# Performance work log

Measured on AMD Instinct MI355X. Metric: run time of the kernel, lower is better.

## Reference

```python
import jax, jax.numpy as jnp
import numpy as np

ZETA = 1.03
GAMMA = -0.03


def setup_inputs() -> dict:
    key = jax.random.key(0)
    k1, k2, k3 = jax.random.split(key, 3)
    B, S, H, D = 2, 2048, 16, 128
    return {
        "query_states": jax.random.normal(k1, (B * S, H, D), dtype=jnp.float32),
        "key_states": jax.random.normal(k2, (B * S, H, D), dtype=jnp.float32),
        "value_states": jax.random.normal(k3, (B * S, H, D), dtype=jnp.float32),
        "batch_size": B,
        "q_length": S,
        "kv_length": S,
    }


def reference(query_states, key_states, value_states, batch_size, q_length, kv_length):
    H = query_states.shape[1]
    D = query_states.shape[2]
    # [B*S, H, D] -> [B, S, H, D]
    q = query_states.reshape(batch_size, q_length, H, D)
    k = key_states.reshape(batch_size, kv_length, H, D)
    v = value_states.reshape(batch_size, kv_length, H, D)
    # scores: [B, H, Q, K]
    scores = jnp.einsum("bqhd,bkhd->bhqk", q, k) / jnp.sqrt(jnp.float32(D)).astype(q.dtype)
    causal = jnp.triu(jnp.ones((q_length, kv_length), dtype=bool), k=1)  # True above diagonal
    scores = jnp.where(causal[None, None, :, :], -jnp.inf, scores)
    probs = jax.nn.softmax(scores, axis=-1)
    # clipped softmax (fp8 recipe): clip((zeta-gamma)*p + gamma, 0, 1)
    probs = jnp.clip((ZETA - GAMMA) * probs + GAMMA, 0.0, 1.0)
    out = jnp.einsum("bhqk,bkhd->bqhd", probs, v)
    return out.reshape(batch_size * q_length, H, D)
```

## Files before the change

kernel.cpp:

```cpp
#include <hip/hip_runtime.h>

typedef __attribute__((ext_vector_type(4))) float f32x4;
typedef __attribute__((ext_vector_type(8))) short bf16x8;
typedef __attribute__((ext_vector_type(4))) int   i32x4;
typedef __attribute__((ext_vector_type(2))) int   i32x2;

#define B_ 2
#define S_ 2048
#define H_ 16
#define D_ 128
#define RS_ (H_ * D_)
#define LOG2E 1.44269504088896340736f
#define ZG 1.06f
#define GM (-0.03f)
#define QSC (0.08838834764831845f * LOG2E)

__device__ __forceinline__ ushort f2bf(float x) {
    uint u = __builtin_bit_cast(uint, x);
    u += 0x7FFFu + ((u >> 16) & 1u);
    return (ushort)(u >> 16);
}

__device__ __forceinline__ void gld16(const void* g, void* l) {
    __builtin_amdgcn_global_load_lds(
        (const __attribute__((address_space(1))) unsigned int*)g,
        (__attribute__((address_space(3))) unsigned int*)l, 16, 0, 0);
}

__global__ __launch_bounds__(256)
void prep_kv(const float* __restrict__ Kg, const float* __restrict__ Vg,
             ushort* __restrict__ Kb, ushort* __restrict__ Vt)
{
    __shared__ ushort Vl[64 * 136];
    const int t = threadIdx.x;
    if (blockIdx.x < 512) {
        const int n  = blockIdx.x;
        const int bh = n >> 4;
        const int ch = n & 15;
        const int s  = ch * 128 + (t >> 1);
        const int d0 = (t & 1) * 64;
        const int b  = bh >> 4, h = bh & 15;
        const float* in = Kg + (((size_t)b * S_ + s) * H_ + h) * D_ + d0;
        ushort* out = Kb + ((size_t)bh * S_ + s) * D_ + d0;
#pragma unroll
        for (int j = 0; j < 4; ++j) {
            f32x4 x0 = *(const f32x4*)(in + j * 16);
            f32x4 x1 = *(const f32x4*)(in + j * 16 + 4);
            f32x4 x2 = *(const f32x4*)(in + j * 16 + 8);
            f32x4 x3 = *(const f32x4*)(in + j * 16 + 12);
            union { ushort u[16]; i32x4 v[2]; } p;
#pragma unroll
            for (int i = 0; i < 4; ++i) {
                p.u[i]      = f2bf(x0[i]);
                p.u[4 + i]  = f2bf(x1[i]);
                p.u[8 + i]  = f2bf(x2[i]);
                p.u[12 + i] = f2bf(x3[i]);
            }
            *(i32x4*)(out + j * 16)     = p.v[0];
            *(i32x4*)(out + j * 16 + 8) = p.v[1];
        }
    } else {
        const int n  = blockIdx.x - 512;
        const int bh = n >> 5;
        const int kt = n & 31;
        const int b  = bh >> 4, h = bh & 15;
#pragma unroll
        for (int it = 0; it < 2; ++it) {
            const int r  = it * 32 + (t >> 3);
            const int c0 = (t & 7) * 16;
            const int s  = kt * 64 + r;
            const float* in = Vg + (((size_t)b * S_ + s) * H_ + h) * D_ + c0;
            f32x4 x0 = *(const f32x4*)(in);
            f32x4 x1 = *(const f32x4*)(in + 4);
            f32x4 x2 = *(const f32x4*)(in + 8);
            f32x4 x3 = *(const f32x4*)(in + 12);
            union { ushort u[16]; i32x4 v[2]; } p;
#pragma unroll
            for (int i = 0; i < 4; ++i) {
                p.u[i]      = f2bf(x0[i]);
                p.u[4 + i]  = f2bf(x1[i]);
                p.u[8 + i]  = f2bf(x2[i]);
                p.u[12 + i] = f2bf(x3[i]);
            }
            *(i32x4*)(Vl + r * 136 + c0)     = p.v[0];
            *(i32x4*)(Vl + r * 136 + c0 + 8) = p.v[1];
        }
        __syncthreads();
        const int d  = t >> 1;
        const int kh = (t & 1) * 32;
        ushort* out = Vt + ((size_t)bh * 32 + kt) * 8192 + d * 64 + kh;
        uint wds[16];
#pragma unroll
        for (int i = 0; i < 16; ++i) {
            uint a = Vl[(kh + 2 * i) * 136 + d];
            uint c = Vl[(kh + 2 * i + 1) * 136 + d];
            wds[i] = a | (c << 16);
        }
#pragma unroll
        for (int j = 0; j < 4; ++j)
            *(i32x4*)(out + j * 8) = *(i32x4*)&wds[j * 4];
    }
}

__global__ __launch_bounds__(256, 3)
void attn_one(const float* __restrict__ Qg, const ushort* __restrict__ Kb,
              const ushort* __restrict__ Vt, float* __restrict__ Og)
{
    __shared__ char SHc[32768 + 4 * 2304 + 4096 + 16];

    const int tid  = threadIdx.x;
    const int w    = tid >> 6;
    const int lane = tid & 63;
    const int g    = lane >> 4;
    const int l15  = lane & 15;
    char*  const Kl    = SHc;
    char*  const Vl    = SHc + 16384;
    char*  const pB    = SHc + 32768 + w * 2304;
    float* const SmaxL = (float*)(SHc + 41984);
    uint*  const Flags = (uint*)(SHc + 46080);

    const int n  = blockIdx.x;
    const int qt = 31 - (n >> 5);
    const int bh = n & 31;
    const int b  = bh >> 4, h = bh & 15;

    const int q0  = qt * 64;
    const int qw0 = q0 + w * 16;
    const int qme = qw0 + l15;

    const float*  Qbh = Qg + ((size_t)b * S_ * H_ + h) * D_;
    const ushort* Kp  = Kb + (size_t)bh * S_ * D_;
    const ushort* Vp  = Vt + (size_t)bh * 32 * 8192;

    auto stageK2 = [&](int kt) {
#pragma unroll
        for (int i = 0; i < 8; ++i) {
            const int u = (w * 8 + i) * 64 + lane;
            const int r = u >> 4, cc = u & 15;
            const ushort* src = Kp + (size_t)(kt * 128 + r) * 128 + ((cc ^ (r & 15)) * 8);
            gld16(src, SHc + (w * 8 + i) * 1024);
        }
    };
    auto stageKV = [&](int kt) {
#pragma unroll
        for (int i = 0; i < 4; ++i) {
            const int u = (w * 4 + i) * 64 + lane;
            const int r = u >> 4, cc = u & 15;
            const ushort* src = Kp + (size_t)(kt * 64 + r) * 128 + ((cc ^ (r & 15)) * 8);
            gld16(src, Kl + (w * 4 + i) * 1024);
        }
        const ushort* tile = Vp + (size_t)kt * 8192;
#pragma unroll
        for (int i = 0; i < 4; ++i) {
            const int u = (w * 4 + i) * 64 + lane;
            const int r = u >> 3, cc = u & 7;
            const ushort* src = tile + r * 64 + ((cc ^ (r & 7)) * 8);
            gld16(src, Vl + (w * 4 + i) * 1024);
        }
    };

    stageK2(0);

    bf16x8 qf[4];
    {
        const float* qptr = Qbh + (size_t)qme * RS_;
#pragma unroll
        for (int db = 0; db < 4; ++db) {
            const float* p = qptr + db * 32 + g * 8;
            f32x4 a = *(const f32x4*)p;
            f32x4 d = *(const f32x4*)(p + 4);
#pragma unroll
            for (int i = 0; i < 4; ++i) {
                qf[db][i]     = (short)f2bf(a[i] * QSC);
                qf[db][i + 4] = (short)f2bf(d[i] * QSC);
            }
        }
    }
    asm volatile("s_waitcnt vmcnt(0)" ::: "memory");
    __syncthreads();

    float acc = 0.f;
    const int kt1 = (q0 + 191) >> 7;
#pragma unroll 1
    for (int kt = 0; kt < kt1; ++kt) {
        const ushort* K2 = (const ushort*)SHc;
        f32x4 s[8];
#pragma unroll
        for (int cc = 0; cc < 8; ++cc) s[cc] = (f32x4){0.f, 0.f, 0.f, 0.f};
        __builtin_amdgcn_s_setprio(1);
#pragma unroll
        for (int db = 0; db < 4; ++db) {
            const int usw = ((db * 4 + g) ^ l15) * 8;
#pragma unroll
            for (int cc = 0; cc < 8; ++cc) {
                bf16x8 kf = *(const bf16x8*)(K2 + (cc * 16 + l15) * 128 + usw);
                s[cc] = __builtin_amdgcn_mfma_f32_16x16x32_bf16(kf, qf[db], s[cc], 0, 0, 0);
            }
        }
        __builtin_amdgcn_s_setprio(0);
        float sm = -1e30f;
        if (kt == kt1 - 1) {
#pragma unroll
            for (int cc = 0; cc < 8; ++cc) {
                const int key0 = kt * 128 + cc * 16 + g * 4;
#pragma unroll
                for (int r = 0; r < 4; ++r) {
                    const bool ok = (key0 + r <= qme);
                    const float e = exp2f(s[cc][r]);
                    acc += ok ? e : 0.f;
                    sm = fmaxf(sm, ok ? s[cc][r] : -1e30f);
                }
            }
        } else {
#pragma unroll
            for (int cc = 0; cc < 8; ++cc)
#pragma unroll
                for (int r = 0; r < 4; ++r) {
                    acc += exp2f(s[cc][r]);
                    sm = fmaxf(sm, s[cc][r]);
                }
        }
        sm = fmaxf(sm, __shfl_xor(sm, 16));
        sm = fmaxf(sm, __shfl_xor(sm, 32));
        if (lane < 16) SmaxL[(w * 16 + kt) * 16 + l15] = sm;
        __syncthreads();
        if (kt + 1 < kt1) {
            stageK2(kt + 1);
            asm volatile("s_waitcnt vmcnt(0)" ::: "memory");
        }
        __syncthreads();
    }

    float c1;
    {
        float t = acc;
        t += __shfl_xor(t, 16);
        t += __shfl_xor(t, 32);
        c1 = ZG / t;
    }
    const float thr = log2f(-GM / c1);

    uint mymask = 0;
#pragma unroll 1
    for (int st = 0; st < kt1; ++st) {
        const float sm = SmaxL[(w * 16 + st) * 16 + l15];
        if (__any(sm > thr)) mymask |= (1u << st);
    }
    if (lane == 0) Flags[w] = mymask;
    __syncthreads();
    const uint blockmask = Flags[0] | Flags[1] | Flags[2] | Flags[3];

    const int kt2 = qt + 1;
    int kt = 0;
    while (kt < kt2 && !((blockmask >> (kt >> 1)) & 1u)) ++kt;
    if (kt < kt2) stageKV(kt);
    asm volatile("s_waitcnt vmcnt(0)" ::: "memory");
    __syncthreads();

    f32x4 o[8];
#pragma unroll
    for (int db = 0; db < 8; ++db) o[db] = (f32x4){0.f, 0.f, 0.f, 0.f};

#pragma unroll 1
    while (kt < kt2) {
        f32x4 s[4];
#pragma unroll
        for (int cb = 0; cb < 4; ++cb) s[cb] = (f32x4){0.f, 0.f, 0.f, 0.f};
        __builtin_amdgcn_s_setprio(1);
#pragma unroll
        for (int db = 0; db < 4; ++db) {
            const int usw = ((db * 4 + g) ^ l15) * 8;
#pragma unroll
            for (int cb = 0; cb < 4; ++cb) {
                bf16x8 kf = *(const bf16x8*)((const ushort*)Kl + (cb * 16 + l15) * 128 + usw);
                s[cb] = __builtin_amdgcn_mfma_f32_16x16x32_bf16(kf, qf[db], s[cb], 0, 0, 0);
            }
        }
        __builtin_amdgcn_s_setprio(0);

        float smax = fmaxf(fmaxf(fmaxf(s[0][0], s[0][1]), fmaxf(s[0][2], s[0][3])),
                           fmaxf(fmaxf(s[1][0], s[1][1]), fmaxf(s[1][2], s[1][3])));
        smax = fmaxf(smax,
               fmaxf(fmaxf(fmaxf(s[2][0], s[2][1]), fmaxf(s[2][2], s[2][3])),
                     fmaxf(fmaxf(s[3][0], s[3][1]), fmaxf(s[3][2], s[3][3]))));

        if (__any(smax > thr)) {
            const bool diag = (kt == kt2 - 1);
#pragma unroll
            for (int cb = 0; cb < 4; ++cb) {
                const int key0 = kt * 64 + cb * 16 + g * 4;
                float p[4];
#pragma unroll
                for (int r = 0; r < 4; ++r) {
                    float e = exp2f(s[cb][r]);
                    if (diag) e = (key0 + r <= qme) ? e : 0.f;
                    p[r] = fminf(fmaxf(c1 * e + GM, 0.f), 1.f);
                }
                uint r01, r23;
                asm("v_cvt_pk_bf16_f32 %0, %1, %2" : "=v"(r01) : "v"(p[0]), "v"(p[1]));
                asm("v_cvt_pk_bf16_f32 %0, %1, %2" : "=v"(r23) : "v"(p[2]), "v"(p[3]));
                i32x2 pv2 = {(int)r01, (int)r23};
                *(i32x2*)(pB + l15 * 144 + cb * 32 + g * 8) = pv2;
            }
            asm volatile("s_waitcnt lgkmcnt(0)" ::: "memory");
            f32x4 onew[8];
            __builtin_amdgcn_s_setprio(1);
#pragma unroll
            for (int ks = 0; ks < 2; ++ks) {
                bf16x8 pf = *(const bf16x8*)(pB + l15 * 144 + ks * 64 + g * 16);
#pragma unroll
                for (int db = 0; db < 8; ++db) {
                    const int d = db * 16 + l15;
                    bf16x8 vf = *(const bf16x8*)(Vl + d * 128 +
                                                 (((ks * 4 + g) ^ (d & 7)) * 16));
                    f32x4& dst = (ks == 0) ? onew[db] : o[db];
                    const f32x4 src = (ks == 0) ? o[db] : onew[db];
                    dst = __builtin_amdgcn_mfma_f32_16x16x32_bf16(pf, vf, src, 0, 0, 0);
                }
            }
            __builtin_amdgcn_s_setprio(0);
        }

        int nkt = kt + 1;
        while (nkt < kt2 && !((blockmask >> (nkt >> 1)) & 1u)) ++nkt;
        __syncthreads();
        if (nkt < kt2) {
            stageKV(nkt);
            asm volatile("s_waitcnt vmcnt(0)" ::: "memory");
        }
        __syncthreads();
        kt = nkt;
    }

    const size_t orow0 = ((size_t)(b * S_ + qw0) * H_ + h) * D_;
#pragma unroll
    for (int db = 0; db < 8; ++db) {
#pragma unroll
        for (int r = 0; r < 4; ++r) {
            const int qr = g * 4 + r;
            Og[orow0 + (size_t)qr * RS_ + db * 16 + l15] = o[db][r];
        }
    }
}

__global__ __launch_bounds__(256, 2)
void attn_fwd(const float* __restrict__ Qg, const float* __restrict__ Kg,
              const float* __restrict__ Vg, float* __restrict__ Og)
{
    __shared__ ushort Kl[32 * 128];
    __shared__ ushort Vt[128 * 40];
    __shared__ ushort Pl[4][16 * 40];

    const int tid  = threadIdx.x;
    const int w    = tid >> 6;
    const int lane = tid & 63;
    const int g    = lane >> 4;
    const int l15  = lane & 15;

    const int q0 = blockIdx.x * 64;
    const int bh = blockIdx.y;
    const int b  = bh >> 4;
    const int h  = bh & (H_ - 1);

    const size_t bh_off = ((size_t)b * S_ * H_ + h) * D_;
    const float* Qp = Qg + bh_off;
    const float* Kp = Kg + bh_off;
    const float* Vp = Vg + bh_off;

    const int qw0 = q0 + w * 16;
    const int wave_last_q = qw0 + 15;
    bf16x8 qf[4];
    {
        const float* qptr = Qp + (size_t)(qw0 + l15) * RS_;
        const float sc = 0.08838834764831845f;
#pragma unroll
        for (int db = 0; db < 4; ++db) {
            const float* p = qptr + db * 32 + g * 8;
            f32x4 a = *(const f32x4*)p;
            f32x4 c = *(const f32x4*)(p + 4);
#pragma unroll
            for (int i = 0; i < 4; ++i) {
                qf[db][i]     = (short)f2bf(a[i] * sc);
                qf[db][i + 4] = (short)f2bf(c[i] * sc);
            }
        }
    }

    char* const klB = (char*)Kl;
    char* const vtB = (char*)Vt;
    const int kr  = tid >> 3;
    const int kcu = (tid & 7) * 2;
    const int vk  = (tid >> 5) * 4;
    const int vd  = (tid & 31) * 4;

    auto stageK = [&](int kt0) {
        const float* p = Kp + (size_t)(kt0 + kr) * RS_ + kcu * 8;
        f32x4 x0 = *(const f32x4*)(p);
        f32x4 x1 = *(const f32x4*)(p + 4);
        f32x4 x2 = *(const f32x4*)(p + 8);
        f32x4 x3 = *(const f32x4*)(p + 12);
        union { ushort u[8]; i32x4 v; } a, c;
#pragma unroll
        for (int i = 0; i < 4; ++i) {
            a.u[i]     = f2bf(x0[i]);
            a.u[i + 4] = f2bf(x1[i]);
            c.u[i]     = f2bf(x2[i]);
            c.u[i + 4] = f2bf(x3[i]);
        }
        const int sw = kr & 7;
        *(i32x4*)(klB + kr * 256 + ((kcu ^ sw) * 16))       = a.v;
        *(i32x4*)(klB + kr * 256 + (((kcu + 1) ^ sw) * 16)) = c.v;
    };

    auto stageV = [&](int kt0) {
        ushort t[4][4];
#pragma unroll
        for (int i = 0; i < 4; ++i) {
            const f32x4 x = *(const f32x4*)(Vp + (size_t)(kt0 + vk + i) * RS_ + vd);
#pragma unroll
            for (int j = 0; j < 4; ++j) t[i][j] = f2bf(x[j]);
        }
#pragma unroll
        for (int j = 0; j < 4; ++j) {
            union { ushort u[4]; i32x2 v; } pk;
#pragma unroll
            for (int i = 0; i < 4; ++i) pk.u[i] = t[i][j];
            *(i32x2*)(vtB + (size_t)(vd + j) * 80 + vk * 2) = pk.v;
        }
    };

    auto qkTile = [&](f32x4& s0, f32x4& s1) {
        s0 = (f32x4){0.f, 0.f, 0.f, 0.f};
        s1 = (f32x4){0.f, 0.f, 0.f, 0.f};
        const int swz = l15 & 7;
#pragma unroll
        for (int db = 0; db < 4; ++db) {
            const int unit = db * 4 + g;
            bf16x8 k0 = *(const bf16x8*)(klB + l15 * 256 + ((unit ^ swz) * 16));
            bf16x8 k1 = *(const bf16x8*)(klB + (l15 + 16) * 256 + ((unit ^ swz) * 16));
            s0 = __builtin_amdgcn_mfma_f32_16x16x32_bf16(qf[db], k0, s0, 0, 0, 0);
            s1 = __builtin_amdgcn_mfma_f32_16x16x32_bf16(qf[db], k1, s1, 0, 0, 0);
        }
    };

    const int ktiles = (q0 + 64) / 32;

    float m[4] = {-1e30f, -1e30f, -1e30f, -1e30f};
    float l[4] = {0.f, 0.f, 0.f, 0.f};

    for (int kt = 0; kt < ktiles; ++kt) {
        const int kt0 = kt * 32;
        __syncthreads();
        stageK(kt0);
        __syncthreads();
        if (kt0 > wave_last_q) continue;
        f32x4 s0, s1;
        qkTile(s0, s1);
#pragma unroll
        for (int r = 0; r < 4; ++r) {
            const int qq = qw0 + g * 4 + r;
            const int ke = kt0 + l15;
            float v0 = (ke <= qq)      ? s0[r] : -1e30f;
            float v1 = (ke + 16 <= qq) ? s1[r] : -1e30f;
            float tmax = fmaxf(v0, v1);
            tmax = fmaxf(tmax, __shfl_xor(tmax, 1));
            tmax = fmaxf(tmax, __shfl_xor(tmax, 2));
            tmax = fmaxf(tmax, __shfl_xor(tmax, 4));
            tmax = fmaxf(tmax, __shfl_xor(tmax, 8));
            const float mn = fmaxf(m[r], tmax);
            float es = exp2f((v0 - mn) * LOG2E) + exp2f((v1 - mn) * LOG2E);
            es += __shfl_xor(es, 1);
            es += __shfl_xor(es, 2);
            es += __shfl_xor(es, 4);
            es += __shfl_xor(es, 8);
            l[r] = l[r] * exp2f((m[r] - mn) * LOG2E) + es;
            m[r] = mn;
        }
    }

    float c1[4];
#pragma unroll
    for (int r = 0; r < 4; ++r) c1[r] = ZG / l[r];

    f32x4 o[8];
#pragma unroll
    for (int db = 0; db < 8; ++db) o[db] = (f32x4){0.f, 0.f, 0.f, 0.f};

    char* const pB = (char*)(Pl[w]);

    for (int kt = 0; kt < ktiles; ++kt) {
        const int kt0 = kt * 32;
        __syncthreads();
        stageK(kt0);
        stageV(kt0);
        __syncthreads();
        if (kt0 > wave_last_q) continue;
        f32x4 s0, s1;
        qkTile(s0, s1);
#pragma unroll
        for (int r = 0; r < 4; ++r) {
            const int qq = qw0 + g * 4 + r;
            const int ke = kt0 + l15;
            float v0 = (ke <= qq)      ? s0[r] : -1e30f;
            float v1 = (ke + 16 <= qq) ? s1[r] : -1e30f;
            float p0 = c1[r] * exp2f((v0 - m[r]) * LOG2E) + GM;
            float p1 = c1[r] * exp2f((v1 - m[r]) * LOG2E) + GM;
            p0 = fminf(fmaxf(p0, 0.f), 1.f);
            p1 = fminf(fmaxf(p1, 0.f), 1.f);
            const int qr = g * 4 + r;
            *(ushort*)(pB + qr * 80 + l15 * 2)        = f2bf(p0);
            *(ushort*)(pB + qr * 80 + (l15 + 16) * 2) = f2bf(p1);
        }
        asm volatile("s_waitcnt lgkmcnt(0)" ::: "memory");
        bf16x8 pf = *(const bf16x8*)(pB + l15 * 80 + g * 16);
#pragma unroll
        for (int db = 0; db < 8; ++db) {
            bf16x8 vf = *(const bf16x8*)(vtB + (size_t)(db * 16 + l15) * 80 + g * 16);
            o[db] = __builtin_amdgcn_mfma_f32_16x16x32_bf16(pf, vf, o[db], 0, 0, 0);
        }
    }

    const size_t orow0 = ((size_t)(b * S_ + qw0) * H_ + h) * D_;
#pragma unroll
    for (int db = 0; db < 8; ++db) {
#pragma unroll
        for (int r = 0; r < 4; ++r) {
            const int qr = g * 4 + r;
            Og[orow0 + (size_t)qr * RS_ + db * 16 + l15] = o[db][r];
        }
    }
}

extern "C" void kernel_launch(void* const* d_in, const int* in_sizes, int n_in,
                              void* d_out, int out_size, void* d_ws, size_t ws_size,
                              hipStream_t stream)
{
    const float* Q = (const float*)d_in[0];
    const float* K = (const float*)d_in[1];
    const float* V = (const float*)d_in[2];
    (void)in_sizes; (void)n_in; (void)out_size;

    if (ws_size >= (size_t)33554432) {
        ushort* Kb = (ushort*)d_ws;
        ushort* Vt = (ushort*)d_ws + 8388608;
        prep_kv<<<dim3(1536), dim3(256), 0, stream>>>(K, V, Kb, Vt);
        attn_one<<<dim3(1024), dim3(256), 0, stream>>>(Q, Kb, Vt, (float*)d_out);
    } else {
        attn_fwd<<<dim3(S_ / 64, B_ * H_), dim3(256), 0, stream>>>(Q, K, V, (float*)d_out);
    }
}
```

Before: 83.45 us.

## Split first-pass QK columns across waves, each wave covering all query rows

Measured after the change: 115.6 us. +38.5%, slower.

```diff
diff --git a/kernel.cpp b/kernel.cpp
--- a/kernel.cpp
+++ b/kernel.cpp
@@ -106,7 +106,7 @@
 void attn_one(const float* __restrict__ Qg, const ushort* __restrict__ Kb,
               const ushort* __restrict__ Vt, float* __restrict__ Og)
 {
-    __shared__ char SHc[32768 + 4 * 2304 + 4096 + 16];
+    __shared__ char SHc[32768 + 4 * 2304 + 4096 + 1024 + 16];
 
     const int tid  = threadIdx.x;
     const int w    = tid >> 6;
@@ -117,7 +117,8 @@
     char*  const Vl    = SHc + 16384;
     char*  const pB    = SHc + 32768 + w * 2304;
     float* const SmaxL = (float*)(SHc + 41984);
-    uint*  const Flags = (uint*)(SHc + 46080);
+    float* const Lpart = (float*)(SHc + 46080);
+    uint*  const Flags = (uint*)(SHc + 47104);
 
     const int n  = blockIdx.x;
     const int qt = 31 - (n >> 5);
@@ -161,9 +162,10 @@
 
     stageK2(0);
 
-    bf16x8 qf[4];
-    {
-        const float* qptr = Qbh + (size_t)qme * RS_;
+    bf16x8 qfA[4][4];
+#pragma unroll
+    for (int qg = 0; qg < 4; ++qg) {
+        const float* qptr = Qbh + (size_t)(q0 + qg * 16 + l15) * RS_;
 #pragma unroll
         for (int db = 0; db < 4; ++db) {
             const float* p = qptr + db * 32 + g * 8;
@@ -171,54 +173,67 @@
             f32x4 d = *(const f32x4*)(p + 4);
 #pragma unroll
             for (int i = 0; i < 4; ++i) {
-                qf[db][i]     = (short)f2bf(a[i] * QSC);
-                qf[db][i + 4] = (short)f2bf(d[i] * QSC);
+                qfA[qg][db][i]     = (short)f2bf(a[i] * QSC);
+                qfA[qg][db][i + 4] = (short)f2bf(d[i] * QSC);
             }
         }
     }
     asm volatile("s_waitcnt vmcnt(0)" ::: "memory");
     __syncthreads();
 
-    float acc = 0.f;
+    float acc[4] = {0.f, 0.f, 0.f, 0.f};
+    const int cc0 = w * 2;
     const int kt1 = (q0 + 191) >> 7;
 #pragma unroll 1
     for (int kt = 0; kt < kt1; ++kt) {
         const ushort* K2 = (const ushort*)SHc;
-        f32x4 s[8];
-#pragma unroll
-        for (int cc = 0; cc < 8; ++cc) s[cc] = (f32x4){0.f, 0.f, 0.f, 0.f};
+        f32x4 s[4][2];
+#pragma unroll
+        for (int qg = 0; qg < 4; ++qg)
+#pragma unroll
+            for (int c2 = 0; c2 < 2; ++c2) s[qg][c2] = (f32x4){0.f, 0.f, 0.f, 0.f};
         __builtin_amdgcn_s_setprio(1);
 #pragma unroll
         for (int db = 0; db < 4; ++db) {
-            const int usw = ((db * 4 + g) ^ l15) * 8;
-#pragma unroll
-            for (int cc = 0; cc < 8; ++cc) {
-                bf16x8 kf = *(const bf16x8*)(K2 + (cc * 16 + l15) * 128 + usw);
-                s[cc] = __builtin_amdgcn_mfma_f32_16x16x32_bf16(kf, qf[db], s[cc], 0, 0, 0);
+#pragma unroll
+            for (int c2 = 0; c2 < 2; ++c2) {
+                const int cc = cc0 + c2;
+                bf16x8 kf = *(const bf16x8*)(K2 + (cc * 16 + l15) * 128 +
+                                             (((db * 4 + g) ^ l15) * 8));
+#pragma unroll
+                for (int qg = 0; qg < 4; ++qg)
+                    s[qg][c2] = __builtin_amdgcn_mfma_f32_16x16x32_bf16(kf, qfA[qg][db], s[qg][c2], 0, 0, 0);
             }
         }
         __builtin_amdgcn_s_setprio(0);
+
         float sm = -1e30f;
         if (kt == kt1 - 1) {
 #pragma unroll
-            for (int cc = 0; cc < 8; ++cc) {
-                const int key0 = kt * 128 + cc * 16 + g * 4;
-#pragma unroll
-                for (int r = 0; r < 4; ++r) {
-                    const bool ok = (key0 + r <= qme);
-                    const float e = exp2f(s[cc][r]);
-                    acc += ok ? e : 0.f;
-                    sm = fmaxf(sm, ok ? s[cc][r] : -1e30f);
+            for (int qg = 0; qg < 4; ++qg) {
+                const int q = q0 + qg * 16 + l15;
+#pragma unroll
+                for (int c2 = 0; c2 < 2; ++c2) {
+                    const int key0 = kt * 128 + (cc0 + c2) * 16 + g * 4;
+#pragma unroll
+                    for (int r = 0; r < 4; ++r) {
+                        const bool ok = (key0 + r <= q);
+                        const float e = exp2f(s[qg][c2][r]);
+                        acc[qg] += ok ? e : 0.f;
+                        sm = fmaxf(sm, ok ? s[qg][c2][r] : -1e30f);
+                    }
                 }
             }
         } else {
 #pragma unroll
-            for (int cc = 0; cc < 8; ++cc)
-#pragma unroll
-                for (int r = 0; r < 4; ++r) {
-                    acc += exp2f(s[cc][r]);
-                    sm = fmaxf(sm, s[cc][r]);
-                }
+            for (int qg = 0; qg < 4; ++qg)
+#pragma unroll
+                for (int c2 = 0; c2 < 2; ++c2)
+#pragma unroll
+                    for (int r = 0; r < 4; ++r) {
+                        acc[qg] += exp2f(s[qg][c2][r]);
+                        sm = fmaxf(sm, s[qg][c2][r]);
+                    }
         }
         sm = fmaxf(sm, __shfl_xor(sm, 16));
         sm = fmaxf(sm, __shfl_xor(sm, 32));
@@ -231,19 +246,43 @@
         __syncthreads();
     }
 
-    float c1;
-    {
-        float t = acc;
+#pragma unroll
+    for (int qg = 0; qg < 4; ++qg) {
+        float t = acc[qg];
         t += __shfl_xor(t, 16);
         t += __shfl_xor(t, 32);
-        c1 = ZG / t;
-    }
+        if (lane < 16) Lpart[(w * 4 + qg) * 16 + l15] = t;
+    }
+
+    bf16x8 qf[4];
+    {
+        const float* qptr = Qbh + (size_t)qme * RS_;
+#pragma unroll
+        for (int db = 0; db < 4; ++db) {
+            const float* p = qptr + db * 32 + g * 8;
+            f32x4 a = *(const f32x4*)p;
+            f32x4 d = *(const f32x4*)(p + 4);
+#pragma unroll
+            for (int i = 0; i < 4; ++i) {
+                qf[db][i]     = (short)f2bf(a[i] * QSC);
+                qf[db][i + 4] = (short)f2bf(d[i] * QSC);
+            }
+        }
+    }
+    __syncthreads();
+
+    const float l = Lpart[(0 * 4 + w) * 16 + l15] + Lpart[(1 * 4 + w) * 16 + l15]
+                  + Lpart[(2 * 4 + w) * 16 + l15] + Lpart[(3 * 4 + w) * 16 + l15];
+    const float c1  = ZG / l;
     const float thr = log2f(-GM / c1);
 
     uint mymask = 0;
 #pragma unroll 1
     for (int st = 0; st < kt1; ++st) {
-        const float sm = SmaxL[(w * 16 + st) * 16 + l15];
+        const float sm = fmaxf(fmaxf(SmaxL[(0 * 16 + st) * 16 + l15],
+                                     SmaxL[(1 * 16 + st) * 16 + l15]),
+                               fmaxf(SmaxL[(2 * 16 + st) * 16 + l15],
+                                     SmaxL[(3 * 16 + st) * 16 + l15]));
         if (__any(sm > thr)) mymask |= (1u << st);
     }
     if (lane == 0) Flags[w] = mymask;
```

## Double-buffer 64-key K tiles in softmax-stats pass with finer skip mask

Applied to the files above, without the earlier changes.

Measured after the change: 83.28 us. About the same (-0.2%).

```diff
diff --git a/kernel.cpp b/kernel.cpp
--- a/kernel.cpp
+++ b/kernel.cpp
@@ -106,7 +106,7 @@
 void attn_one(const float* __restrict__ Qg, const ushort* __restrict__ Kb,
               const ushort* __restrict__ Vt, float* __restrict__ Og)
 {
-    __shared__ char SHc[32768 + 4 * 2304 + 4096 + 16];
+    __shared__ char SHc[32768 + 4 * 2304 + 8192 + 16];
 
     const int tid  = threadIdx.x;
     const int w    = tid >> 6;
@@ -117,7 +117,7 @@
     char*  const Vl    = SHc + 16384;
     char*  const pB    = SHc + 32768 + w * 2304;
     float* const SmaxL = (float*)(SHc + 41984);
-    uint*  const Flags = (uint*)(SHc + 46080);
+    uint*  const Flags = (uint*)(SHc + 50176);
 
     const int n  = blockIdx.x;
     const int qt = 31 - (n >> 5);
@@ -132,13 +132,13 @@
     const ushort* Kp  = Kb + (size_t)bh * S_ * D_;
     const ushort* Vp  = Vt + (size_t)bh * 32 * 8192;
 
-    auto stageK2 = [&](int kt) {
-#pragma unroll
-        for (int i = 0; i < 8; ++i) {
-            const int u = (w * 8 + i) * 64 + lane;
+    auto stageK64 = [&](int kt, int bset) {
+#pragma unroll
+        for (int i = 0; i < 4; ++i) {
+            const int u = (w * 4 + i) * 64 + lane;
             const int r = u >> 4, cc = u & 15;
-            const ushort* src = Kp + (size_t)(kt * 128 + r) * 128 + ((cc ^ (r & 15)) * 8);
-            gld16(src, SHc + (w * 8 + i) * 1024);
+            const ushort* src = Kp + (size_t)(kt * 64 + r) * 128 + ((cc ^ (r & 15)) * 8);
+            gld16(src, SHc + bset * 16384 + (w * 4 + i) * 1024);
         }
     };
     auto stageKV = [&](int kt) {
@@ -159,7 +159,7 @@
         }
     };
 
-    stageK2(0);
+    stageK64(0, 0);
 
     bf16x8 qf[4];
     {
@@ -180,55 +180,55 @@
     __syncthreads();
 
     float acc = 0.f;
-    const int kt1 = (q0 + 191) >> 7;
+    const int ktN = qt + 1;
+    int cur = 0;
 #pragma unroll 1
-    for (int kt = 0; kt < kt1; ++kt) {
-        const ushort* K2 = (const ushort*)SHc;
-        f32x4 s[8];
-#pragma unroll
-        for (int cc = 0; cc < 8; ++cc) s[cc] = (f32x4){0.f, 0.f, 0.f, 0.f};
+    for (int kt = 0; kt < ktN; ++kt) {
+        if (kt + 1 < ktN) stageK64(kt + 1, cur ^ 1);
+        const ushort* K1 = (const ushort*)(SHc + cur * 16384);
+        f32x4 s[4];
+#pragma unroll
+        for (int cb = 0; cb < 4; ++cb) s[cb] = (f32x4){0.f, 0.f, 0.f, 0.f};
         __builtin_amdgcn_s_setprio(1);
 #pragma unroll
         for (int db = 0; db < 4; ++db) {
             const int usw = ((db * 4 + g) ^ l15) * 8;
 #pragma unroll
-            for (int cc = 0; cc < 8; ++cc) {
-                bf16x8 kf = *(const bf16x8*)(K2 + (cc * 16 + l15) * 128 + usw);
-                s[cc] = __builtin_amdgcn_mfma_f32_16x16x32_bf16(kf, qf[db], s[cc], 0, 0, 0);
+            for (int cb = 0; cb < 4; ++cb) {
+                bf16x8 kf = *(const bf16x8*)(K1 + (cb * 16 + l15) * 128 + usw);
+                s[cb] = __builtin_amdgcn_mfma_f32_16x16x32_bf16(kf, qf[db], s[cb], 0, 0, 0);
             }
         }
         __builtin_amdgcn_s_setprio(0);
+
         float sm = -1e30f;
-        if (kt == kt1 - 1) {
-#pragma unroll
-            for (int cc = 0; cc < 8; ++cc) {
-                const int key0 = kt * 128 + cc * 16 + g * 4;
+        if (kt == ktN - 1) {
+#pragma unroll
+            for (int cb = 0; cb < 4; ++cb) {
+                const int key0 = kt * 64 + cb * 16 + g * 4;
 #pragma unroll
                 for (int r = 0; r < 4; ++r) {
                     const bool ok = (key0 + r <= qme);
-                    const float e = exp2f(s[cc][r]);
+                    const float e = exp2f(s[cb][r]);
                     acc += ok ? e : 0.f;
-                    sm = fmaxf(sm, ok ? s[cc][r] : -1e30f);
+                    sm = fmaxf(sm, ok ? s[cb][r] : -1e30f);
                 }
             }
         } else {
 #pragma unroll
-            for (int cc = 0; cc < 8; ++cc)
+            for (int cb = 0; cb < 4; ++cb)
 #pragma unroll
                 for (int r = 0; r < 4; ++r) {
-                    acc += exp2f(s[cc][r]);
-                    sm = fmaxf(sm, s[cc][r]);
+                    acc += exp2f(s[cb][r]);
+                    sm = fmaxf(sm, s[cb][r]);
                 }
         }
         sm = fmaxf(sm, __shfl_xor(sm, 16));
         sm = fmaxf(sm, __shfl_xor(sm, 32));
-        if (lane < 16) SmaxL[(w * 16 + kt) * 16 + l15] = sm;
-        __syncthreads();
-        if (kt + 1 < kt1) {
-            stageK2(kt + 1);
-            asm volatile("s_waitcnt vmcnt(0)" ::: "memory");
-        }
-        __syncthreads();
+        if (lane < 16) SmaxL[(w * 32 + kt) * 16 + l15] = sm;
+        asm volatile("s_waitcnt vmcnt(0)" ::: "memory");
+        __syncthreads();
+        cur ^= 1;
     }
 
     float c1;
@@ -242,8 +242,8 @@
 
     uint mymask = 0;
 #pragma unroll 1
-    for (int st = 0; st < kt1; ++st) {
-        const float sm = SmaxL[(w * 16 + st) * 16 + l15];
+    for (int st = 0; st < ktN; ++st) {
+        const float sm = SmaxL[(w * 32 + st) * 16 + l15];
         if (__any(sm > thr)) mymask |= (1u << st);
     }
     if (lane == 0) Flags[w] = mymask;
@@ -252,7 +252,7 @@
 
     const int kt2 = qt + 1;
     int kt = 0;
-    while (kt < kt2 && !((blockmask >> (kt >> 1)) & 1u)) ++kt;
+    while (kt < kt2 && !((blockmask >> kt) & 1u)) ++kt;
     if (kt < kt2) stageKV(kt);
     asm volatile("s_waitcnt vmcnt(0)" ::: "memory");
     __syncthreads();
@@ -322,7 +322,7 @@
         }
 
         int nkt = kt + 1;
-        while (nkt < kt2 && !((blockmask >> (nkt >> 1)) & 1u)) ++nkt;
+        while (nkt < kt2 && !((blockmask >> nkt) & 1u)) ++nkt;
         __syncthreads();
         if (nkt < kt2) {
             stageKV(nkt);
```
